# Optimization experiments

Measured on AMD Instinct MI355X. Metric: run time of the kernel, lower is better.

Reference implementation:

```python
import jax, jax.numpy as jnp
import numpy as np

B, S, D, H = 2, 2048, 1024, 16
DK = D // H


def setup_inputs() -> dict:
    key = jax.random.key(0)
    ks = jax.random.split(key, 7)
    return {
        "query": jax.random.normal(ks[0], (B, S, D), jnp.float32),
        "key": jax.random.normal(ks[1], (B, S, D), jnp.float32),
        "value": jax.random.normal(ks[2], (B, S, D), jnp.float32),
        "w_q": jax.random.normal(ks[3], (D, D), jnp.float32) * (1.0 / np.sqrt(D)),
        "w_k": jax.random.normal(ks[4], (D, D), jnp.float32) * (1.0 / np.sqrt(D)),
        "w_v": jax.random.normal(ks[5], (D, D), jnp.float32) * (1.0 / np.sqrt(D)),
        "w_o": jax.random.normal(ks[6], (D, D), jnp.float32) * (1.0 / np.sqrt(D)),
    }


def reference(query, key, value, w_q, w_k, w_v, w_o):
    # Linear(bias=False) in torch computes x @ W.T where W is [out, in].
    Q = jnp.einsum('bsd,ed->bse', query, w_q)
    K = jnp.einsum('bsd,ed->bse', key, w_k)
    V = jnp.einsum('bsd,ed->bse', value, w_v)
    # split heads: [B, H, S, DK]
    Q = Q.reshape(B, S, H, DK).transpose(0, 2, 1, 3)
    K = K.reshape(B, S, H, DK).transpose(0, 2, 1, 3)
    V = V.reshape(B, S, H, DK).transpose(0, 2, 1, 3)
    scale = 1.0 / np.sqrt(DK).astype(np.float32)
    scores = jnp.einsum('bhqd,bhkd->bhqk', Q, K) * scale  # [B,H,S,S]
    attn = jax.nn.softmax(scores, axis=-1)
    context = jnp.einsum('bhqk,bhkd->bhqd', attn, V)
    context = context.transpose(0, 2, 1, 3).reshape(B, S, D)
    return jnp.einsum('bsd,ed->bse', context, w_o)
```

## Files before the change

### kernel.cpp

```cpp
#include <hip/hip_runtime.h>

typedef unsigned short u16;
typedef unsigned int u32;
typedef __bf16 bf16x8 __attribute__((ext_vector_type(8)));
typedef float f32x4 __attribute__((ext_vector_type(4)));
typedef short s16x4 __attribute__((ext_vector_type(4)));

#define AS1 __attribute__((address_space(1)))
#define AS3 __attribute__((address_space(3)))

__device__ __forceinline__ f32x4 mfma16(bf16x8 a, bf16x8 b, f32x4 c) {
    return __builtin_amdgcn_mfma_f32_16x16x32_bf16(a, b, c, 0, 0, 0);
}
__device__ __forceinline__ f32x4 mfma16k16(s16x4 a, s16x4 b, f32x4 c) {
    return __builtin_amdgcn_mfma_f32_16x16x16bf16_1k(a, b, c, 0, 0, 0);
}

__device__ __forceinline__ u16 f2bf(float f) {
    return __builtin_bit_cast(u16, (__bf16)f);
}

__device__ __forceinline__ void gld16(const u16* g, u16* l) {
    __builtin_amdgcn_global_load_lds((AS1 void*)g, (AS3 void*)l, 16, 0, 0);
}

__global__ __launch_bounds__(256) void cvt_all(const float* __restrict__ q, const float* __restrict__ k,
                                               const float* __restrict__ v, const float* __restrict__ wq,
                                               const float* __restrict__ wk, const float* __restrict__ wv,
                                               const float* __restrict__ wo, u16* __restrict__ qo,
                                               u16* __restrict__ ko, u16* __restrict__ vo,
                                               u16* __restrict__ wqo, u16* __restrict__ wko,
                                               u16* __restrict__ wvo, u16* __restrict__ woo) {
    const int y = blockIdx.y;
    const float* x; u16* o; int n;
    switch (y) {
        case 0: x = q; o = qo; n = 4 << 20; break;
        case 1: x = k; o = ko; n = 4 << 20; break;
        case 2: x = v; o = vo; n = 4 << 20; break;
        case 3: x = wq; o = wqo; n = 1 << 20; break;
        case 4: x = wk; o = wko; n = 1 << 20; break;
        case 5: x = wv; o = wvo; n = 1 << 20; break;
        default: x = wo; o = woo; n = 1 << 20; break;
    }
    int i = (blockIdx.x * 256 + threadIdx.x) * 4;
    if (i >= n) return;
    float4 vv = *(const float4*)(x + i);
    u32 lo = (u32)f2bf(vv.x) | ((u32)f2bf(vv.y) << 16);
    u32 hi = (u32)f2bf(vv.z) | ((u32)f2bf(vv.w) << 16);
    *(uint2*)(o + i) = make_uint2(lo, hi);
}

template <int BM, int BN, bool BF16OUT>
__device__ __forceinline__ void gemm_core(const u16* __restrict__ A, const u16* __restrict__ Bt,
                                          void* __restrict__ Cp, int K, int N, int m0, int n0,
                                          float oscale) {
    constexpr int WROWS = BM / 64;
    constexpr int WCOLS = 4 / WROWS;
    constexpr int BFR = BN / WCOLS / 16;
    __shared__ __align__(16) u16 As[BM * 32];
    __shared__ __align__(16) u16 Bs[BN * 32];
    const int tid = threadIdx.x;
    const int lane = tid & 63, wave = tid >> 6;
    const int l16 = lane & 15, q4 = lane >> 4;
    const int wm = (wave / WCOLS) * 64, wn = (wave % WCOLS) * (BFR * 16);

    const f32x4 fz = {0.f, 0.f, 0.f, 0.f};
    f32x4 acc[4][BFR];
#pragma unroll
    for (int i = 0; i < 4; ++i)
#pragma unroll
        for (int j = 0; j < BFR; ++j) acc[i][j] = fz;

    const int rseg = lane >> 2;
    const int ck = ((lane & 3) ^ ((lane >> 3) & 3)) * 8;
    const u16* Ag = A + (size_t)(m0 + wave * 16 + rseg) * K + ck;
    const u16* Bg = Bt + (size_t)(n0 + wave * 16 + rseg) * K + ck;

    const int swz = (q4 ^ ((l16 & 7) >> 1)) * 8;

    for (int k0 = 0; k0 < K; k0 += 32) {
        __syncthreads();
#pragma unroll
        for (int p = 0; p < BM / 64; ++p)
            gld16(Ag + (size_t)p * 64 * K + k0, As + p * 2048 + wave * 512);
#pragma unroll
        for (int p = 0; p < BN / 64; ++p)
            gld16(Bg + (size_t)p * 64 * K + k0, Bs + p * 2048 + wave * 512);
        __syncthreads();
        bf16x8 af[4], bfr[BFR];
#pragma unroll
        for (int i = 0; i < 4; ++i)
            af[i] = *(const bf16x8*)&As[(wm + i * 16 + l16) * 32 + swz];
#pragma unroll
        for (int j = 0; j < BFR; ++j)
            bfr[j] = *(const bf16x8*)&Bs[(wn + j * 16 + l16) * 32 + swz];
#pragma unroll
        for (int i = 0; i < 4; ++i)
#pragma unroll
            for (int j = 0; j < BFR; ++j) acc[i][j] = mfma16(af[i], bfr[j], acc[i][j]);
    }

#pragma unroll
    for (int i = 0; i < 4; ++i) {
        const int row = m0 + wm + i * 16 + q4 * 4;
#pragma unroll
        for (int j = 0; j < BFR; ++j) {
            const int col = n0 + wn + j * 16 + l16;
#pragma unroll
            for (int r = 0; r < 4; ++r) {
                const float vr = acc[i][j][r] * oscale;
                if constexpr (BF16OUT)
                    ((u16*)Cp)[(size_t)(row + r) * N + col] = f2bf(vr);
                else
                    ((float*)Cp)[(size_t)(row + r) * N + col] = vr;
            }
        }
    }
}

__global__ __launch_bounds__(256) void gemm_qkv(const u16* __restrict__ qb, const u16* __restrict__ kb,
                                                const u16* __restrict__ vb, const u16* __restrict__ wqb,
                                                const u16* __restrict__ wkb, const u16* __restrict__ wvb,
                                                u16* __restrict__ Qp, u16* __restrict__ Kp,
                                                u16* __restrict__ VtAll) {
    const int z = blockIdx.y, x = blockIdx.x;
    const u16 *A, *Bt;
    u16* C;
    int N, m0, n0;
    float sc = 1.0f;
    if (z == 0) {
        A = qb; Bt = wqb; C = Qp; N = 1024; m0 = (x >> 3) * 128; n0 = (x & 7) * 128;
        sc = 0.18033688011112042f;
    } else if (z == 1) {
        A = kb; Bt = wkb; C = Kp; N = 1024; m0 = (x >> 3) * 128; n0 = (x & 7) * 128;
    } else {
        A = wvb; Bt = vb; C = VtAll; N = 4096; m0 = (x >> 5) * 128; n0 = (x & 31) * 128;
    }
    gemm_core<128, 128, true>(A, Bt, C, 1024, N, m0, n0, sc);
}

__global__ __launch_bounds__(256) void gemm_out(const u16* __restrict__ ctx,
                                                const u16* __restrict__ wob,
                                                float* __restrict__ out) {
    const int x = blockIdx.x;
    gemm_core<64, 128, false>(ctx, wob, out, 1024, 1024, (x >> 3) * 64, (x & 7) * 128, 1.0f);
}

__global__ __launch_bounds__(256) void flash_attn(const u16* __restrict__ Qp,
                                                  const u16* __restrict__ Kp,
                                                  const u16* __restrict__ VtAll,
                                                  u16* __restrict__ Ctx) {
    constexpr int D = 1024, SS = 2048, LD = 72;
    __shared__ __align__(16) u16 Ks[2][64 * LD];
    __shared__ __align__(16) u16 Vts[2][64 * LD];

    const int tid = threadIdx.x;
    const int lane = tid & 63, wave = tid >> 6;
    const int l16 = lane & 15, q4 = lane >> 4;
    const int h = blockIdx.y, b = blockIdx.z;
    const int q0 = blockIdx.x * 128 + wave * 32;

    bf16x8 qf[2][2];
#pragma unroll
    for (int qs = 0; qs < 2; ++qs) {
        const u16* Qb = Qp + (size_t)(b * SS + q0 + qs * 16 + l16) * D + h * 64;
        qf[qs][0] = *(const bf16x8*)(Qb + q4 * 8);
        qf[qs][1] = *(const bf16x8*)(Qb + 32 + q4 * 8);
    }

    const f32x4 fz = {0.f, 0.f, 0.f, 0.f};
    f32x4 ot[2][4], lacc[2];
    lacc[0] = fz; lacc[1] = fz;
#pragma unroll
    for (int qs = 0; qs < 2; ++qs)
#pragma unroll
        for (int dt = 0; dt < 4; ++dt) ot[qs][dt] = fz;

    s16x4 onesA;
    onesA[0] = onesA[1] = onesA[2] = onesA[3] = (short)0x3F80;

    const int sr = tid >> 3, scol = (tid & 7) * 8;
    const int vswap = wave & 1;
    const int swV = (l16 >> 3) & 1;
    const u16* Kg = Kp + (size_t)(b * SS + sr) * D + h * 64 + scol;
    const u16* Vg = VtAll + (size_t)(h * 64 + sr) * 4096 + b * SS + scol;

    uint4 k0v = *(const uint4*)(Kg);
    uint4 k1v = *(const uint4*)(Kg + (size_t)32 * D);
    uint4 v0v = *(const uint4*)(Vg);
    uint4 v1v = *(const uint4*)(Vg + (size_t)32 * 4096);

    for (int kt = 0; kt < SS; kt += 64) {
        const int buf = (kt >> 6) & 1;
        uint4 w0 = v0v, w1 = v1v;
        if (vswap) {
            w0 = make_uint4(v0v.z, v0v.w, v0v.x, v0v.y);
            w1 = make_uint4(v1v.z, v1v.w, v1v.x, v1v.y);
        }
        *(uint4*)&Ks[buf][sr * LD + scol] = k0v;
        *(uint4*)&Ks[buf][(sr + 32) * LD + scol] = k1v;
        *(uint4*)&Vts[buf][sr * LD + scol] = w0;
        *(uint4*)&Vts[buf][(sr + 32) * LD + scol] = w1;

        const int nk = (kt + 64 < SS) ? kt + 64 : 0;
        k0v = *(const uint4*)(Kg + (size_t)nk * D);
        k1v = *(const uint4*)(Kg + (size_t)(nk + 32) * D);
        v0v = *(const uint4*)(Vg + nk);
        v1v = *(const uint4*)(Vg + (size_t)32 * 4096 + nk);

        __syncthreads();

        f32x4 st[2][4];
#pragma unroll
        for (int nt = 0; nt < 4; ++nt) {
            const bf16x8 ka = *(const bf16x8*)&Ks[buf][(nt * 16 + l16) * LD + q4 * 8];
            const bf16x8 kbf = *(const bf16x8*)&Ks[buf][(nt * 16 + l16) * LD + 32 + q4 * 8];
#pragma unroll
            for (int qs = 0; qs < 2; ++qs) {
                f32x4 s = mfma16(ka, qf[qs][0], fz);
                st[qs][nt] = mfma16(kbf, qf[qs][1], s);
            }
        }
        s16x4 p[2][4];
#pragma unroll
        for (int qs = 0; qs < 2; ++qs)
#pragma unroll
            for (int nt = 0; nt < 4; ++nt) {
                s16x4 pk;
#pragma unroll
                for (int r = 0; r < 4; ++r)
                    pk[r] = (short)f2bf(__builtin_amdgcn_exp2f(st[qs][nt][r]));
                p[qs][nt] = pk;
            }
#pragma unroll
        for (int nt = 0; nt < 4; ++nt) {
#pragma unroll
            for (int dt = 0; dt < 4; ++dt) {
                const s16x4 va =
                    *(const s16x4*)&Vts[buf][(dt * 16 + l16) * LD + ((nt * 4 + q4) ^ swV) * 4];
                ot[0][dt] = mfma16k16(va, p[0][nt], ot[0][dt]);
                ot[1][dt] = mfma16k16(va, p[1][nt], ot[1][dt]);
            }
            lacc[0] = mfma16k16(onesA, p[0][nt], lacc[0]);
            lacc[1] = mfma16k16(onesA, p[1][nt], lacc[1]);
        }
    }

#pragma unroll
    for (int qs = 0; qs < 2; ++qs) {
        const float inv = 1.f / lacc[qs][0];
        u16* Cb = Ctx + (size_t)(b * SS + q0 + qs * 16 + l16) * D + h * 64 + q4 * 4;
#pragma unroll
        for (int dt = 0; dt < 4; ++dt) {
            s16x4 w;
#pragma unroll
            for (int r = 0; r < 4; ++r) w[r] = (short)f2bf(ot[qs][dt][r] * inv);
            *(s16x4*)(Cb + dt * 16) = w;
        }
    }
}

extern "C" void kernel_launch(void* const* d_in, const int* in_sizes, int n_in,
                              void* d_out, int out_size, void* d_ws, size_t ws_size,
                              hipStream_t stream) {
    const float* query = (const float*)d_in[0];
    const float* key   = (const float*)d_in[1];
    const float* value = (const float*)d_in[2];
    const float* w_q   = (const float*)d_in[3];
    const float* w_k   = (const float*)d_in[4];
    const float* w_v   = (const float*)d_in[5];
    const float* w_o   = (const float*)d_in[6];
    float* out = (float*)d_out;

    const size_t MEG = 1024 * 1024;
    if (ws_size < 64 * MEG) return;
    u16* ws = (u16*)d_ws;
    u16* qb    = ws;
    u16* kb    = ws + 4 * MEG;
    u16* vb    = ws + 8 * MEG;
    u16* wqb   = ws + 12 * MEG;
    u16* wkb   = ws + 13 * MEG;
    u16* wvb   = ws + 14 * MEG;
    u16* wob   = ws + 15 * MEG;
    u16* Qp    = ws + 16 * MEG;
    u16* Kp    = ws + 20 * MEG;
    u16* VtAll = ws + 24 * MEG;
    u16* ctx   = ws + 28 * MEG;

    cvt_all<<<dim3(4096, 7), 256, 0, stream>>>(query, key, value, w_q, w_k, w_v, w_o,
                                               qb, kb, vb, wqb, wkb, wvb, wob);
    gemm_qkv<<<dim3(256, 3), 256, 0, stream>>>(qb, kb, vb, wqb, wkb, wvb, Qp, Kp, VtAll);
    flash_attn<<<dim3(16, 16, 2), 256, 0, stream>>>(Qp, Kp, VtAll, ctx);
    gemm_out<<<dim3(512), 256, 0, stream>>>(ctx, wob, out);
}
```

Baseline: 217.3 us.

## Stream K via async global-to-LDS loads and read V fragments directly from global

K tiles now move into a swizzled, unpadded LDS double buffer through global_load_lds, with the next tile prefetched right after the barrier, so the register staging and separate LDS store step go away. V no longer goes through LDS at all: each lane loads its s16x4 MFMA fragments straight from the transposed V in global memory every iteration. This cuts LDS traffic and footprint, but V loads become small 8-byte global reads that rely on the cache, and their latency is no longer hidden by a prefetch.

```diff
diff --git a/kernel.cpp b/kernel.cpp
--- a/kernel.cpp
+++ b/kernel.cpp
@@ -150,9 +150,8 @@
                                                   const u16* __restrict__ Kp,
                                                   const u16* __restrict__ VtAll,
                                                   u16* __restrict__ Ctx) {
-    constexpr int D = 1024, SS = 2048, LD = 72;
-    __shared__ __align__(16) u16 Ks[2][64 * LD];
-    __shared__ __align__(16) u16 Vts[2][64 * LD];
+    constexpr int D = 1024, SS = 2048;
+    __shared__ __align__(16) u16 Ks[2][64 * 64];
 
     const int tid = threadIdx.x;
     const int lane = tid & 63, wave = tid >> 6;
@@ -179,42 +178,40 @@
     s16x4 onesA;
     onesA[0] = onesA[1] = onesA[2] = onesA[3] = (short)0x3F80;
 
-    const int sr = tid >> 3, scol = (tid & 7) * 8;
-    const int vswap = wave & 1;
-    const int swV = (l16 >> 3) & 1;
-    const u16* Kg = Kp + (size_t)(b * SS + sr) * D + h * 64 + scol;
-    const u16* Vg = VtAll + (size_t)(h * 64 + sr) * 4096 + b * SS + scol;
-
-    uint4 k0v = *(const uint4*)(Kg);
-    uint4 k1v = *(const uint4*)(Kg + (size_t)32 * D);
-    uint4 v0v = *(const uint4*)(Vg);
-    uint4 v1v = *(const uint4*)(Vg + (size_t)32 * 4096);
+    const int sr = tid >> 3;
+    const int ck = ((lane & 7) ^ (lane >> 3)) * 8;
+    const u16* Kg = Kp + (size_t)(b * SS + sr) * D + h * 64 + ck;
+    const int ldsW = wave * 512;
+
+    const u16* Vlane = VtAll + (size_t)(h * 64 + l16) * 4096 + (size_t)b * SS + q4 * 4;
+
+    gld16(Kg, (u16*)Ks[0] + ldsW);
+    gld16(Kg + (size_t)32 * D, (u16*)Ks[0] + ldsW + 2048);
+
+    const int pos = (q4 ^ (l16 & 7)) * 8;
 
     for (int kt = 0; kt < SS; kt += 64) {
         const int buf = (kt >> 6) & 1;
-        uint4 w0 = v0v, w1 = v1v;
-        if (vswap) {
-            w0 = make_uint4(v0v.z, v0v.w, v0v.x, v0v.y);
-            w1 = make_uint4(v1v.z, v1v.w, v1v.x, v1v.y);
-        }
-        *(uint4*)&Ks[buf][sr * LD + scol] = k0v;
-        *(uint4*)&Ks[buf][(sr + 32) * LD + scol] = k1v;
-        *(uint4*)&Vts[buf][sr * LD + scol] = w0;
-        *(uint4*)&Vts[buf][(sr + 32) * LD + scol] = w1;
-
-        const int nk = (kt + 64 < SS) ? kt + 64 : 0;
-        k0v = *(const uint4*)(Kg + (size_t)nk * D);
-        k1v = *(const uint4*)(Kg + (size_t)(nk + 32) * D);
-        v0v = *(const uint4*)(Vg + nk);
-        v1v = *(const uint4*)(Vg + (size_t)32 * 4096 + nk);
-
         __syncthreads();
+        if (kt + 64 < SS) {
+            const u16* Kn = Kg + (size_t)(kt + 64) * D;
+            gld16(Kn, (u16*)Ks[buf ^ 1] + ldsW);
+            gld16(Kn + (size_t)32 * D, (u16*)Ks[buf ^ 1] + ldsW + 2048);
+        }
+
+        s16x4 vf[4][4];
+#pragma unroll
+        for (int dt = 0; dt < 4; ++dt)
+#pragma unroll
+            for (int nt = 0; nt < 4; ++nt)
+                vf[dt][nt] = *(const s16x4*)(Vlane + (size_t)dt * 16 * 4096 + kt + nt * 16);
 
         f32x4 st[2][4];
 #pragma unroll
         for (int nt = 0; nt < 4; ++nt) {
-            const bf16x8 ka = *(const bf16x8*)&Ks[buf][(nt * 16 + l16) * LD + q4 * 8];
-            const bf16x8 kbf = *(const bf16x8*)&Ks[buf][(nt * 16 + l16) * LD + 32 + q4 * 8];
+            const int R = (nt * 16 + l16) * 64;
+            const bf16x8 ka = *(const bf16x8*)&Ks[buf][R + pos];
+            const bf16x8 kbf = *(const bf16x8*)&Ks[buf][R + (pos ^ 32)];
 #pragma unroll
             for (int qs = 0; qs < 2; ++qs) {
                 f32x4 s = mfma16(ka, qf[qs][0], fz);
@@ -236,10 +233,8 @@
         for (int nt = 0; nt < 4; ++nt) {
 #pragma unroll
             for (int dt = 0; dt < 4; ++dt) {
-                const s16x4 va =
-                    *(const s16x4*)&Vts[buf][(dt * 16 + l16) * LD + ((nt * 4 + q4) ^ swV) * 4];
-                ot[0][dt] = mfma16k16(va, p[0][nt], ot[0][dt]);
-                ot[1][dt] = mfma16k16(va, p[1][nt], ot[1][dt]);
+                ot[0][dt] = mfma16k16(vf[dt][nt], p[0][nt], ot[0][dt]);
+                ot[1][dt] = mfma16k16(vf[dt][nt], p[1][nt], ot[1][dt]);
             }
             lacc[0] = mfma16k16(onesA, p[0][nt], lacc[0]);
             lacc[1] = mfma16k16(onesA, p[1][nt], lacc[1]);
```

New measurement: 285.1 us. +31.2%, slower.
